# Kernel optimization log

Hardware: AMD Instinct MI355X
Metric: run time of the kernel (lower is better)

The kernel has to match this reference:

```python
import jax, jax.numpy as jnp
import numpy as np

B, S, D, H, K = 8, 1024, 512, 512, 8  # batch, seq, input_dim, hidden, max neighbors


def setup_inputs() -> dict:
    key = jax.random.key(0)
    ks = jax.random.split(key, 10)
    p = lambda k, shape: (0.05 * jax.random.normal(k, shape, jnp.float32))
    return {
        "input_t": jax.random.normal(ks[0], (B, S, D), jnp.float32),
        "comb_idx": jax.random.randint(ks[1], (B, S, K), 0, S, jnp.int32),
        "comb_mask": jax.random.randint(ks[2], (B, S, K), 0, 2, jnp.int32),
        "order": jnp.arange(B, dtype=jnp.int64),
        # PyTorch LSTM params per direction; b = b_ih + b_hh fused (mathematically identical)
        "w_ih_f": p(ks[3], (4 * H, D)),
        "w_hh_f": p(ks[4], (4 * H, H)),
        "b_f": p(ks[5], (4 * H,)),
        "w_ih_b": p(ks[6], (4 * H, D)),
        "w_hh_b": p(ks[7], (4 * H, H)),
        "b_b": p(ks[8], (4 * H,)),
    }


def _lstm_scan(x_sbd, w_ih, w_hh, b, reverse):
    # x_sbd: [S, B, D]; PyTorch gate order i, f, g, o; zero initial state (inithidden)
    Bb = x_sbd.shape[1]
    Hh = w_hh.shape[1]
    h0 = jnp.zeros((Bb, Hh), x_sbd.dtype)
    c0 = jnp.zeros((Bb, Hh), x_sbd.dtype)

    def cell(carry, xt):
        h, c = carry
        z = xt @ w_ih.T + h @ w_hh.T + b
        i, f, g, o = jnp.split(z, 4, axis=-1)
        c = jax.nn.sigmoid(f) * c + jax.nn.sigmoid(i) * jnp.tanh(g)
        h = jax.nn.sigmoid(o) * jnp.tanh(c)
        return (h, c), h

    (hn, cn), hs = jax.lax.scan(cell, (h0, c0), x_sbd, reverse=reverse)
    return hs, hn, cn  # hs in original time order even when reverse=True


def reference(input_t, comb_idx, comb_mask, order, w_ih_f, w_hh_f, b_f, w_ih_b, w_hh_b, b_b):
    x = jnp.swapaxes(input_t, 0, 1)  # [S, B, D]
    hs_f, hn_f, cn_f = _lstm_scan(x, w_ih_f, w_hh_f, b_f, reverse=False)
    hs_b, hn_b, cn_b = _lstm_scan(x, w_ih_b, w_hh_b, b_b, reverse=True)
    padded = jnp.swapaxes(jnp.concatenate([hs_f, hs_b], axis=-1), 0, 1)  # [B, S, 2H]
    h_n = jnp.stack([hn_f, hn_b])  # [2, B, H]
    c_n = jnp.stack([cn_f, cn_b])

    # comb = batch_comb[order[idx]]
    ci = comb_idx[order]                                  # [B, S, K]
    cm = comb_mask[order].astype(padded.dtype)            # [B, S, K]
    gathered = jax.vmap(lambda xb, ib: xb[ib])(padded, ci)  # [B, S, K, 2H]
    neigh_sum = (gathered * cm[..., None]).sum(axis=2)    # [B, S, 2H]
    cnt = cm.sum(axis=-1)                                 # [B, S]
    rep = (padded + neigh_sum) / (1.0 + cnt)[..., None]   # (x_i + sum_j x_j) / (|comb_i| + 1)
    rep = rep[:, 1:-1, :]                                 # drop first/last token

    # reorder_batch_encoder_rep[order[i]] = rep[i]
    out = jnp.zeros_like(rep).at[order].set(rep)
    return out, h_n, c_n
```

## Files before the change

### kernel.cpp

```cpp
#include <hip/hip_runtime.h>
#include <stdint.h>

typedef unsigned short u16;
typedef unsigned long long u64;
typedef __attribute__((ext_vector_type(8))) short short8v;
typedef __attribute__((ext_vector_type(4))) float f32x4;

#define OUT_HN   8372224
#define OUT_CN   8380416

#define WS_FLAGS 0
#define WS_CSB   4096
#define WS_HSB0  36864
#define WS_HSB1  8433664
#define WS_ZX    16830464

__device__ __forceinline__ u16 f2bf(float f) {
  uint32_t u = __float_as_uint(f);
  u += 0x7FFFu + ((u >> 16) & 1u);
  return (u16)(u >> 16);
}
__device__ __forceinline__ float bf2f(u16 v) {
  return __uint_as_float(((uint32_t)v) << 16);
}
__device__ __forceinline__ short8v cvt8(const float* p) {
  float4 a = *(const float4*)p;
  float4 b = *(const float4*)(p + 4);
  short8v r;
  r[0] = (short)f2bf(a.x); r[1] = (short)f2bf(a.y);
  r[2] = (short)f2bf(a.z); r[3] = (short)f2bf(a.w);
  r[4] = (short)f2bf(b.x); r[5] = (short)f2bf(b.y);
  r[6] = (short)f2bf(b.z); r[7] = (short)f2bf(b.w);
  return r;
}

__global__ void k_init(uint32_t* flags) {
  if (threadIdx.x < 64) flags[threadIdx.x] = 0;
}

__global__ void k_zero(u16* h0, u16* h1, float* c) {
  int i = blockIdx.x * blockDim.x + threadIdx.x;
  if (i < 4096) { h0[i] = 0; h1[i] = 0; }
  if (i < 8192) c[i] = 0.f;
}

#define STAGE_X(tcol)                                                          \
  {                                                                            \
    _Pragma("unroll")                                                          \
    for (int half = 0; half < 2; ++half) {                                     \
      int g = tid + half * 256;                                                \
      int r = g >> 6, B = g & 63;                                              \
      const float* xr = xf + ((size_t)r * 1024 + (tcol)) * 512 + B * 8;        \
      float4 a = *(const float4*)xr;                                           \
      float4 b = *(const float4*)(xr + 4);                                     \
      short8v v;                                                               \
      v[0] = (short)f2bf(a.x); v[1] = (short)f2bf(a.y);                        \
      v[2] = (short)f2bf(a.z); v[3] = (short)f2bf(a.w);                        \
      v[4] = (short)f2bf(b.x); v[5] = (short)f2bf(b.y);                        \
      v[6] = (short)f2bf(b.z); v[7] = (short)f2bf(b.w);                        \
      *(short8v*)(xL + r * 512 + ((B ^ r) << 3)) = v;                          \
    }                                                                          \
  }

__global__ void k_zx(const float* __restrict__ xf,
                     const float* __restrict__ wihf, const float* __restrict__ wihb,
                     u16* __restrict__ zx, int s0, int seglen)
{
  const int nch  = seglen >> 5;
  const int bid  = blockIdx.x;
  const int chunk = bid % nch;
  const int wg   = (bid / nch) & 15;
  const int dir  = bid / (nch * 16);
  const int tid  = threadIdx.x;
  const int wid  = tid >> 6;
  const int lane = tid & 63;
  const int jbase = wg * 32;
  const float* wih = dir ? wihb : wihf;

  __shared__ u16 xL[8 * 512];
  __shared__ float zL[4 * 8 * 32];

  short8v bih[2][16];
  {
    const int rr = lane & 15;
    const int ko = (lane >> 4) * 8;
    #pragma unroll
    for (int nt = 0; nt < 2; ++nt) {
      const int row = wid * 512 + jbase + nt * 16 + rr;
      #pragma unroll
      for (int kt = 0; kt < 16; ++kt)
        bih[nt][kt] = cvt8(wih + (size_t)row * 512 + kt * 32 + ko);
    }
  }

  const int rB = lane & 7;
  const int q  = lane >> 4;
  const f32x4 fzero = {0.f, 0.f, 0.f, 0.f};

  for (int i = 0; i < 32; ++i) {
    const int sidx = chunk * 32 + i;
    const int gstep = s0 + sidx;
    const int tn = dir ? (1023 - gstep) : gstep;
    STAGE_X(tn);
    __syncthreads();
    f32x4 acc0 = fzero, acc1 = fzero;
    #pragma unroll
    for (int kt = 0; kt < 16; ++kt) {
      short8v ax = *(const short8v*)(xL + rB * 512 + (((kt * 4 + q) ^ rB) << 3));
      acc0 = __builtin_amdgcn_mfma_f32_16x16x32_bf16(ax, bih[0][kt], acc0, 0, 0, 0);
      acc1 = __builtin_amdgcn_mfma_f32_16x16x32_bf16(ax, bih[1][kt], acc1, 0, 0, 0);
    }
    if (lane < 32) {
      #pragma unroll
      for (int r = 0; r < 4; ++r) {
        const int brow = (lane >> 4) * 4 + r;
        zL[wid * 256 + brow * 32 + (lane & 15)]      = acc0[r];
        zL[wid * 256 + brow * 32 + 16 + (lane & 15)] = acc1[r];
      }
    }
    __syncthreads();
    if (tid < 128) {
      const int b = tid >> 4;
      const int r = (tid & 15) * 8;
      const int g = r >> 5;
      const int jj = r & 31;
      short8v v;
      #pragma unroll
      for (int w = 0; w < 8; ++w) v[w] = (short)f2bf(zL[g * 256 + b * 32 + jj + w]);
      *(short8v*)(zx + (((size_t)dir * seglen + sidx) * 16 + wg) * 1024 + tid * 8) = v;
    }
    __syncthreads();
  }
}

__launch_bounds__(256, 1)
__global__ void k_lstm(const float* __restrict__ whhf, const float* __restrict__ whhb,
                       const float* __restrict__ bias0, const float* __restrict__ bias1,
                       const u16* __restrict__ zx,
                       u16* hsb0, u16* hsb1, float* csb, float* out,
                       uint32_t* flags, int s0, int s1, int seglen)
{
  const int tid  = threadIdx.x;
  const int wid  = tid >> 6;
  const int lane = tid & 63;
  const int dir  = blockIdx.x >> 4;
  const int wg   = blockIdx.x & 15;
  const int jbase = wg * 32;

  const float* whh  = dir ? whhb : whhf;
  const float* bias = dir ? bias1 : bias0;
  u16* hsb = dir ? hsb1 : hsb0;
  uint32_t* fl = flags + dir * 16;

  __shared__ u16 hL[8 * 512];
  __shared__ float zL[4 * 8 * 32];
  __shared__ u16 hS[8 * 32];
  __shared__ u64 zxL[256];

  short8v bhh[2][16];
  {
    const int rr = lane & 15;
    const int ko = (lane >> 4) * 8;
    #pragma unroll
    for (int nt = 0; nt < 2; ++nt) {
      const int row = wid * 512 + jbase + nt * 16 + rr;
      #pragma unroll
      for (int kt = 0; kt < 16; ++kt)
        bhh[nt][kt] = cvt8(whh + (size_t)row * 512 + kt * 32 + ko);
    }
  }

  const int cb = tid >> 5;
  const int cj = tid & 31;
  const float bz0 = bias[0 * 512 + jbase + cj];
  const float bz1 = bias[1 * 512 + jbase + cj];
  const float bz2 = bias[2 * 512 + jbase + cj];
  const float bz3 = bias[3 * 512 + jbase + cj];
  float* cp = csb + dir * 4096 + cb * 512 + jbase + cj;
  float c_state = *cp;

  const int rB = lane & 7;
  const int q  = lane >> 4;
  const f32x4 fzero = {0.f, 0.f, 0.f, 0.f};
  const u16* zx16 = (const u16*)zxL;

  for (int gstep = s0; gstep < s1; ++gstep) {
    {
      const u64* zp = (const u64*)(zx + (((size_t)dir * seglen + (gstep - s0)) * 16 + wg) * 1024);
      zxL[tid] = zp[tid];
    }
    if (tid < 16) {
      int guard = 0;
      while (__hip_atomic_load(&fl[tid], __ATOMIC_RELAXED, __HIP_MEMORY_SCOPE_AGENT)
             < (uint32_t)gstep && ++guard < (1 << 15)) { }
    }
    __syncthreads();
    {
      const u64* hc = (const u64*)(hsb + (size_t)gstep * 4096);
      u64 d0 = __hip_atomic_load(hc + 4 * tid + 0, __ATOMIC_RELAXED, __HIP_MEMORY_SCOPE_AGENT);
      u64 d1 = __hip_atomic_load(hc + 4 * tid + 1, __ATOMIC_RELAXED, __HIP_MEMORY_SCOPE_AGENT);
      u64 d2 = __hip_atomic_load(hc + 4 * tid + 2, __ATOMIC_RELAXED, __HIP_MEMORY_SCOPE_AGENT);
      u64 d3 = __hip_atomic_load(hc + 4 * tid + 3, __ATOMIC_RELAXED, __HIP_MEMORY_SCOPE_AGENT);
      union { u64 qq[2]; short8v v; } p0, p1;
      p0.qq[0] = d0; p0.qq[1] = d1;
      p1.qq[0] = d2; p1.qq[1] = d3;
      int G0 = 2 * tid, G1 = 2 * tid + 1;
      int r0 = G0 >> 6, B0 = G0 & 63;
      int r1 = G1 >> 6, B1 = G1 & 63;
      *(short8v*)(hL + r0 * 512 + ((B0 ^ r0) << 3)) = p0.v;
      *(short8v*)(hL + r1 * 512 + ((B1 ^ r1) << 3)) = p1.v;
    }
    __syncthreads();
    f32x4 acc0 = fzero, acc1 = fzero;
    #pragma unroll
    for (int kt = 0; kt < 16; ++kt) {
      short8v ah = *(const short8v*)(hL + rB * 512 + (((kt * 4 + q) ^ rB) << 3));
      acc0 = __builtin_amdgcn_mfma_f32_16x16x32_bf16(ah, bhh[0][kt], acc0, 0, 0, 0);
      acc1 = __builtin_amdgcn_mfma_f32_16x16x32_bf16(ah, bhh[1][kt], acc1, 0, 0, 0);
    }
    if (lane < 32) {
      #pragma unroll
      for (int r = 0; r < 4; ++r) {
        const int brow = (lane >> 4) * 4 + r;
        zL[wid * 256 + brow * 32 + (lane & 15)]      = acc0[r];
        zL[wid * 256 + brow * 32 + 16 + (lane & 15)] = acc1[r];
      }
    }
    __syncthreads();
    {
      float zi = zL[0 * 256 + cb * 32 + cj] + bz0 + bf2f(zx16[cb * 128 +  0 + cj]);
      float zf = zL[1 * 256 + cb * 32 + cj] + bz1 + bf2f(zx16[cb * 128 + 32 + cj]);
      float zg = zL[2 * 256 + cb * 32 + cj] + bz2 + bf2f(zx16[cb * 128 + 64 + cj]);
      float zo = zL[3 * 256 + cb * 32 + cj] + bz3 + bf2f(zx16[cb * 128 + 96 + cj]);
      float si = 1.f / (1.f + __expf(-zi));
      float sf = 1.f / (1.f + __expf(-zf));
      float so = 1.f / (1.f + __expf(-zo));
      float ag = fabsf(zg); float eg = __expf(-2.f * ag);
      float tg = (1.f - eg) / (1.f + eg); tg = copysignf(tg, zg);
      c_state = sf * c_state + si * tg;
      float ac = fabsf(c_state); float ec = __expf(-2.f * ac);
      float tc = (1.f - ec) / (1.f + ec); tc = copysignf(tc, c_state);
      float h = so * tc;
      hS[cb * 32 + cj] = f2bf(h);
      if (gstep == 1023) {
        out[OUT_HN + dir * 4096 + cb * 512 + jbase + cj] = h;
        out[OUT_CN + dir * 4096 + cb * 512 + jbase + cj] = c_state;
      }
    }
    __syncthreads();
    if (tid < 64) {
      const int pb = tid >> 3;
      const int pt = tid & 7;
      u64 hv = *(const u64*)(hS + pb * 32 + 4 * pt);
      u64* dst = (u64*)(hsb + ((size_t)(gstep + 1) * 8 + pb) * 512 + jbase + 4 * pt);
      __hip_atomic_store(dst, hv, __ATOMIC_RELAXED, __HIP_MEMORY_SCOPE_AGENT);
      asm volatile("s_waitcnt vmcnt(0)" ::: "memory");
    }
    if (tid == 0) {
      __hip_atomic_store(&fl[wg], (uint32_t)(gstep + 1), __ATOMIC_RELAXED,
                         __HIP_MEMORY_SCOPE_AGENT);
    }
  }
  *cp = c_state;
}

__global__ void k_combine(const u16* __restrict__ hsb0, const u16* __restrict__ hsb1,
                          const int* __restrict__ cidx, const int* __restrict__ cmask,
                          const int* __restrict__ order, float* __restrict__ out)
{
  const int tid = threadIdx.x;
  const int b = blockIdx.x / 1022;
  const int s = 1 + (blockIdx.x % 1022);
  __shared__ int sidx[8];
  __shared__ float smask[8];
  __shared__ int rsh;
  if (tid == 0) rsh = order[b];
  __syncthreads();
  const int r = rsh;
  if (tid < 8) {
    size_t base = ((size_t)r * 1024 + s) * 8 + tid;
    sidx[tid] = cidx[base];
    smask[tid] = (float)cmask[base];
  }
  __syncthreads();
  float cnt = 0.f;
  #pragma unroll
  for (int k = 0; k < 8; ++k) cnt += smask[k];
  const float inv = 1.f / (1.f + cnt);

  const int col0 = tid * 4;
  const bool isF = col0 < 512;
  const int cloc = isF ? col0 : col0 - 512;
  const u16* hb = isF ? hsb0 : hsb1;

  float v0, v1, v2, v3;
  {
    size_t ci2 = isF ? (size_t)(s + 1) : (size_t)(1024 - s);
    ushort4 qv = *(const ushort4*)(hb + (ci2 * 8 + b) * 512 + cloc);
    v0 = bf2f(qv.x); v1 = bf2f(qv.y); v2 = bf2f(qv.z); v3 = bf2f(qv.w);
  }
  #pragma unroll
  for (int k = 0; k < 8; ++k) {
    float m = smask[k];
    if (m != 0.f) {
      int sp = sidx[k];
      size_t ci2 = isF ? (size_t)(sp + 1) : (size_t)(1024 - sp);
      ushort4 qv = *(const ushort4*)(hb + (ci2 * 8 + b) * 512 + cloc);
      v0 += m * bf2f(qv.x); v1 += m * bf2f(qv.y); v2 += m * bf2f(qv.z); v3 += m * bf2f(qv.w);
    }
  }
  size_t ob = ((size_t)r * 1022 + (s - 1)) * 1024 + col0;
  float4 ov; ov.x = v0 * inv; ov.y = v1 * inv; ov.z = v2 * inv; ov.w = v3 * inv;
  *(float4*)(out + ob) = ov;
}

extern "C" void kernel_launch(void* const* d_in, const int* in_sizes, int n_in,
                              void* d_out, int out_size, void* d_ws, size_t ws_size,
                              hipStream_t stream)
{
  const float* x      = (const float*)d_in[0];
  const int*   cidx   = (const int*)d_in[1];
  const int*   cmask  = (const int*)d_in[2];
  const int*   order  = (const int*)d_in[3];
  const float* wihf = (const float*)d_in[4];
  const float* whhf = (const float*)d_in[5];
  const float* bf   = (const float*)d_in[6];
  const float* wihb = (const float*)d_in[7];
  const float* whhb = (const float*)d_in[8];
  const float* bb   = (const float*)d_in[9];
  float* out = (float*)d_out;

  char* ws = (char*)d_ws;
  uint32_t* FLAGS = (uint32_t*)(ws + WS_FLAGS);
  float* CSB = (float*)(ws + WS_CSB);
  u16* HSB0 = (u16*)(ws + WS_HSB0);
  u16* HSB1 = (u16*)(ws + WS_HSB1);
  u16* ZX   = (u16*)(ws + WS_ZX);

  const int seglen = (ws_size >= (size_t)WS_ZX + 1024ull * 65536) ? 1024 : 128;

  hipLaunchKernelGGL(k_init, dim3(1), dim3(64), 0, stream, FLAGS);
  hipLaunchKernelGGL(k_zero, dim3(32), dim3(256), 0, stream, HSB0, HSB1, CSB);

  for (int s0 = 0; s0 < 1024; s0 += seglen) {
    hipLaunchKernelGGL(k_zx, dim3(2 * 16 * (seglen >> 5)), dim3(256), 0, stream,
                       x, wihf, wihb, ZX, s0, seglen);
    hipLaunchKernelGGL(k_lstm, dim3(32), dim3(256), 0, stream,
                       whhf, whhb, bf, bb, ZX, HSB0, HSB1, CSB, out, FLAGS,
                       s0, s0 + seglen, seglen);
  }

  hipLaunchKernelGGL(k_combine, dim3(8 * 1022), dim3(256), 0, stream,
                     HSB0, HSB1, cidx, cmask, order, out);
}
```

Measured before the change: 2.974 ms.

## Replace per-step flag polling with data-embedded ready bits in hidden-state buffer

```diff
diff --git a/kernel.cpp b/kernel.cpp
--- a/kernel.cpp
+++ b/kernel.cpp
@@ -34,14 +34,16 @@
   return r;
 }
 
-__global__ void k_init(uint32_t* flags) {
-  if (threadIdx.x < 64) flags[threadIdx.x] = 0;
-}
-
-__global__ void k_zero(u16* h0, u16* h1, float* c) {
-  int i = blockIdx.x * blockDim.x + threadIdx.x;
-  if (i < 4096) { h0[i] = 0; h1[i] = 0; }
-  if (i < 8192) c[i] = 0.f;
+__global__ void k_zero(u64* h0, u64* h1, float* c) {
+  const size_t n = 8396800 / 8;
+  const size_t stride = (size_t)gridDim.x * blockDim.x;
+  for (size_t i = (size_t)blockIdx.x * blockDim.x + threadIdx.x; i < n; i += stride) {
+    u64 v = (i < 512) ? 1ull : 0ull;
+    h0[i] = v;
+    h1[i] = v;
+  }
+  int j = blockIdx.x * blockDim.x + threadIdx.x;
+  if (j < 8192) c[j] = 0.f;
 }
 
 #define STAGE_X(tcol)                                                          \
@@ -138,7 +140,7 @@
                        const float* __restrict__ bias0, const float* __restrict__ bias1,
                        const u16* __restrict__ zx,
                        u16* hsb0, u16* hsb1, float* csb, float* out,
-                       uint32_t* flags, int s0, int s1, int seglen)
+                       int s0, int s1, int seglen)
 {
   const int tid  = threadIdx.x;
   const int wid  = tid >> 6;
@@ -150,11 +152,10 @@
   const float* whh  = dir ? whhb : whhf;
   const float* bias = dir ? bias1 : bias0;
   u16* hsb = dir ? hsb1 : hsb0;
-  uint32_t* fl = flags + dir * 16;
 
   __shared__ u16 hL[8 * 512];
   __shared__ float zL[4 * 8 * 32];
-  __shared__ u16 hS[8 * 32];
+  __shared__ u64 hSq[64];
   __shared__ u64 zxL[256];
 
   short8v bhh[2][16];
@@ -183,24 +184,26 @@
   const int q  = lane >> 4;
   const f32x4 fzero = {0.f, 0.f, 0.f, 0.f};
   const u16* zx16 = (const u16*)zxL;
+  u16* hS = (u16*)hSq;
 
   for (int gstep = s0; gstep < s1; ++gstep) {
     {
       const u64* zp = (const u64*)(zx + (((size_t)dir * seglen + (gstep - s0)) * 16 + wg) * 1024);
       zxL[tid] = zp[tid];
     }
-    if (tid < 16) {
-      int guard = 0;
-      while (__hip_atomic_load(&fl[tid], __ATOMIC_RELAXED, __HIP_MEMORY_SCOPE_AGENT)
-             < (uint32_t)gstep && ++guard < (1 << 15)) { }
-    }
-    __syncthreads();
+    u64 d0, d1, d2, d3;
     {
       const u64* hc = (const u64*)(hsb + (size_t)gstep * 4096);
-      u64 d0 = __hip_atomic_load(hc + 4 * tid + 0, __ATOMIC_RELAXED, __HIP_MEMORY_SCOPE_AGENT);
-      u64 d1 = __hip_atomic_load(hc + 4 * tid + 1, __ATOMIC_RELAXED, __HIP_MEMORY_SCOPE_AGENT);
-      u64 d2 = __hip_atomic_load(hc + 4 * tid + 2, __ATOMIC_RELAXED, __HIP_MEMORY_SCOPE_AGENT);
-      u64 d3 = __hip_atomic_load(hc + 4 * tid + 3, __ATOMIC_RELAXED, __HIP_MEMORY_SCOPE_AGENT);
+      int guard = 0;
+      for (;;) {
+        d0 = __hip_atomic_load(hc + 4 * tid + 0, __ATOMIC_RELAXED, __HIP_MEMORY_SCOPE_AGENT);
+        d1 = __hip_atomic_load(hc + 4 * tid + 1, __ATOMIC_RELAXED, __HIP_MEMORY_SCOPE_AGENT);
+        d2 = __hip_atomic_load(hc + 4 * tid + 2, __ATOMIC_RELAXED, __HIP_MEMORY_SCOPE_AGENT);
+        d3 = __hip_atomic_load(hc + 4 * tid + 3, __ATOMIC_RELAXED, __HIP_MEMORY_SCOPE_AGENT);
+        if (((d0 & d1 & d2 & d3) & 1ull) || ++guard >= (1 << 15)) break;
+      }
+    }
+    {
       union { u64 qq[2]; short8v v; } p0, p1;
       p0.qq[0] = d0; p0.qq[1] = d1;
       p1.qq[0] = d2; p1.qq[1] = d3;
@@ -251,14 +254,9 @@
     if (tid < 64) {
       const int pb = tid >> 3;
       const int pt = tid & 7;
-      u64 hv = *(const u64*)(hS + pb * 32 + 4 * pt);
+      u64 hv = hSq[pb * 8 + pt] | 1ull;
       u64* dst = (u64*)(hsb + ((size_t)(gstep + 1) * 8 + pb) * 512 + jbase + 4 * pt);
       __hip_atomic_store(dst, hv, __ATOMIC_RELAXED, __HIP_MEMORY_SCOPE_AGENT);
-      asm volatile("s_waitcnt vmcnt(0)" ::: "memory");
-    }
-    if (tid == 0) {
-      __hip_atomic_store(&fl[wg], (uint32_t)(gstep + 1), __ATOMIC_RELAXED,
-                         __HIP_MEMORY_SCOPE_AGENT);
     }
   }
   *cp = c_state;
@@ -331,7 +329,6 @@
   float* out = (float*)d_out;
 
   char* ws = (char*)d_ws;
-  uint32_t* FLAGS = (uint32_t*)(ws + WS_FLAGS);
   float* CSB = (float*)(ws + WS_CSB);
   u16* HSB0 = (u16*)(ws + WS_HSB0);
   u16* HSB1 = (u16*)(ws + WS_HSB1);
@@ -339,14 +336,14 @@
 
   const int seglen = (ws_size >= (size_t)WS_ZX + 1024ull * 65536) ? 1024 : 128;
 
-  hipLaunchKernelGGL(k_init, dim3(1), dim3(64), 0, stream, FLAGS);
-  hipLaunchKernelGGL(k_zero, dim3(32), dim3(256), 0, stream, HSB0, HSB1, CSB);
+  hipLaunchKernelGGL(k_zero, dim3(1024), dim3(256), 0, stream,
+                     (u64*)HSB0, (u64*)HSB1, CSB);
 
   for (int s0 = 0; s0 < 1024; s0 += seglen) {
     hipLaunchKernelGGL(k_zx, dim3(2 * 16 * (seglen >> 5)), dim3(256), 0, stream,
                        x, wihf, wihb, ZX, s0, seglen);
     hipLaunchKernelGGL(k_lstm, dim3(32), dim3(256), 0, stream,
-                       whhf, whhb, bf, bb, ZX, HSB0, HSB1, CSB, out, FLAGS,
+                       whhf, whhb, bf, bb, ZX, HSB0, HSB1, CSB, out,
                        s0, s0 + seglen, seglen);
   }
 
```

After: 7.448 ms. +150.5%, slower.
